# Optimization experiments

Measured on AMD Instinct MI355X. Metric: run time of the kernel, lower is better.

The kernel has to match this reference:

```python
import jax, jax.numpy as jnp
import numpy as np

EPS = 1e-6

def _rmsnorm(x, w):
    # RMSNorm in float32 as in the torch module, then rescale by weight
    xf = x.astype(jnp.float32)
    y = xf * jax.lax.rsqrt(jnp.mean(xf * xf, axis=-1, keepdims=True) + EPS)
    return y.astype(x.dtype) * w

def setup_inputs() -> dict:
    key = jax.random.key(0)
    k0, k1, k2 = jax.random.split(key, 3)
    B, T, C = 2, 1024, 256
    x = jax.random.normal(k0, (B, T, C), jnp.float32)
    w_qkv = jax.random.normal(k1, (3 * C, C), jnp.float32) / np.float32(np.sqrt(C))
    w_proj = jax.random.normal(k2, (C, C), jnp.float32) / np.float32(np.sqrt(C))
    qn_w = jnp.ones((2,), jnp.float32)
    kn_w = jnp.ones((2,), jnp.float32)
    return {"x": x, "w_qkv": w_qkv, "w_proj": w_proj, "qn_w": qn_w, "kn_w": kn_w}

def reference(x, w_qkv, w_proj, qn_w, kn_w):
    B, T, C = x.shape
    HD = 2                      # head_dim forced to 2 by GPTConfig invariant
    H = C // HD                 # n_head = n_embd // 2
    qkv = x @ w_qkv.T           # (B, T, 3C); Linear has bias=False
    q, k, v = jnp.split(qkv, 3, axis=-1)
    heads = lambda t: t.reshape(B, T, H, HD).transpose(0, 2, 1, 3)  # (B,H,T,2)
    q = _rmsnorm(heads(q), qn_w)
    k = _rmsnorm(heads(k), kn_w)
    v = heads(v)
    scale = np.float32(1.0 / np.sqrt(HD))
    att = jnp.einsum('bhtd,bhsd->bhts', q, k) * scale   # (B,H,T,T)
    causal = jnp.tril(jnp.ones((T, T), bool))
    att = jnp.where(causal, att, jnp.float32(-1e30))
    att = jax.nn.softmax(att, axis=-1)
    y = jnp.einsum('bhts,bhsd->bhtd', att, v)           # (B,H,T,2)
    y = y.transpose(0, 2, 1, 3).reshape(B, T, C)
    return y @ w_proj.T
```

## Files before the change

kernel.cpp:

```cpp
#include <hip/hip_runtime.h>

#define T_SEQ   1024
#define C_DIM   256
#define H_HEADS 128
#define NTOK    2048
#define BH      256
#define NBLK    1024

#define MAGIC1  0x1357ACE5u
#define MAGIC2  0x2468BD17u

typedef unsigned short u16;
typedef unsigned int   u32;
typedef __attribute__((ext_vector_type(8))) short bf16x8;
typedef __attribute__((ext_vector_type(4))) float f32x4;
typedef __attribute__((ext_vector_type(2))) float f32x2;
typedef __attribute__((ext_vector_type(2))) unsigned int u32x2;

__device__ __forceinline__ float bf2f(u16 u) {
  return __uint_as_float(((u32)u) << 16);
}
__device__ __forceinline__ u16 f2bf(float f) {
  u32 u = __float_as_uint(f);
  u32 r = u + 0x7fffu + ((u >> 16) & 1u);
  return (u16)(r >> 16);
}

__device__ __forceinline__ void stwt2(void* p, f32x2 v) {
  asm volatile("global_store_dwordx2 %0, %1, off sc0 sc1" :: "v"(p), "v"(v) : "memory");
}
__device__ __forceinline__ void stwt2u(void* p, u32x2 v) {
  asm volatile("global_store_dwordx2 %0, %1, off sc0 sc1" :: "v"(p), "v"(v) : "memory");
}

__device__ __forceinline__ bf16x8 ldsf(const u16* plane, int row, int kk) {
  int off = (row * 128 + kk * 2) ^ ((row & 7) << 4);
  return *(const bf16x8*)((const char*)plane + off);
}
__device__ __forceinline__ void cvt_store(float4 g, u16* hp, int lo_u16,
                                          int r, int c4) {
  ushort4 h4, l4;
  h4.x = f2bf(g.x); l4.x = f2bf(g.x - bf2f(h4.x));
  h4.y = f2bf(g.y); l4.y = f2bf(g.y - bf2f(h4.y));
  h4.z = f2bf(g.z); l4.z = f2bf(g.z - bf2f(h4.z));
  h4.w = f2bf(g.w); l4.w = f2bf(g.w - bf2f(h4.w));
  int off = (r * 128 + c4 * 2) ^ ((r & 7) << 4);
  *(ushort4*)((char*)hp + off) = h4;
  *(ushort4*)((char*)(hp + lo_u16) + off) = l4;
}

#define AG __HIP_MEMORY_SCOPE_AGENT
__device__ __forceinline__ void slot_set(u32* s, u32 v) {
  __hip_atomic_store(s, v, __ATOMIC_RELAXED, AG);
}
__device__ __forceinline__ u32 slot_get(const u32* s) {
  return __hip_atomic_load(s, __ATOMIC_RELAXED, AG);
}

__device__ __forceinline__ void attn_unit(
    char* smem, const float* __restrict__ q, const float* __restrict__ kk,
    const float* __restrict__ vv, u32* __restrict__ yP,
    int head, int g, int tid, int lane, int w)
{
  float4* skA = (float4*)smem;
  float4* skB = (float4*)(smem + 8192);
  float (*red)[256][3] = (float (*)[256][3])(smem + 16384);

  const int qb = g * 256;
  const int S  = qb + 256;

  {
    const float4* kh = (const float4*)(kk + head * (T_SEQ * 2));
    const float4* vh = (const float4*)(vv + head * (T_SEQ * 2));
    for (int i = tid; i < (S >> 1); i += 256) {
      float4 k4 = kh[i];
      float4 v4 = vh[i];
      skA[i] = make_float4(k4.x, k4.z, k4.y, k4.w);
      skB[i] = make_float4(v4.x, v4.z, v4.y, v4.w);
    }
  }

  const float LS = 0.70710678118f * 1.44269504089f;
  f32x2 qxb[4], qyb[4];
  int   tq[4];
#pragma unroll
  for (int j = 0; j < 4; ++j) {
    int t = qb + j * 64 + lane;
    tq[j] = t;
    float2 qv = *(const float2*)&q[(head * T_SEQ + t) * 2];
    float sx = qv.x * LS, sy = qv.y * LS;
    qxb[j] = (f32x2){sx, sx};
    qyb[j] = (f32x2){sy, sy};
  }
  __syncthreads();

  f32x2 denp[4] = {}, nxp[4] = {}, nyp[4] = {};

  const int cbp = qb >> 3;
  const int p0 = w * cbp, p1 = p0 + cbp;
  for (int p = p0; p < p1; p += 4) {
    float4 A0 = skA[p],     V0 = skB[p];
    float4 A1 = skA[p + 1], V1 = skB[p + 1];
    float4 A2 = skA[p + 2], V2 = skB[p + 2];
    float4 A3 = skA[p + 3], V3 = skB[p + 3];
#pragma unroll
    for (int u = 0; u < 4; ++u) {
      float4 A = (u == 0) ? A0 : (u == 1) ? A1 : (u == 2) ? A2 : A3;
      float4 V = (u == 0) ? V0 : (u == 1) ? V1 : (u == 2) ? V2 : V3;
      f32x2 kx = {A.x, A.y}, ky = {A.z, A.w};
      f32x2 vx = {V.x, V.y}, vy = {V.z, V.w};
#pragma unroll
      for (int j = 0; j < 4; ++j) {
        f32x2 sp = __builtin_elementwise_fma(qxb[j], kx, qyb[j] * ky);
        f32x2 ep = { __builtin_amdgcn_exp2f(sp.x), __builtin_amdgcn_exp2f(sp.y) };
        denp[j] += ep;
        nxp[j] = __builtin_elementwise_fma(ep, vx, nxp[j]);
        nyp[j] = __builtin_elementwise_fma(ep, vy, nyp[j]);
      }
    }
  }
  const int dp0 = (qb >> 1) + w * 32;
  for (int p = dp0; p < dp0 + 32; p += 4) {
    float4 A0 = skA[p],     V0 = skB[p];
    float4 A1 = skA[p + 1], V1 = skB[p + 1];
    float4 A2 = skA[p + 2], V2 = skB[p + 2];
    float4 A3 = skA[p + 3], V3 = skB[p + 3];
#pragma unroll
    for (int u = 0; u < 4; ++u) {
      float4 A = (u == 0) ? A0 : (u == 1) ? A1 : (u == 2) ? A2 : A3;
      float4 V = (u == 0) ? V0 : (u == 1) ? V1 : (u == 2) ? V2 : V3;
      f32x2 kx = {A.x, A.y}, ky = {A.z, A.w};
      f32x2 vx = {V.x, V.y}, vy = {V.z, V.w};
      const int s0 = 2 * (p + u);
#pragma unroll
      for (int j = 0; j < 4; ++j) {
        f32x2 sp = __builtin_elementwise_fma(qxb[j], kx, qyb[j] * ky);
        f32x2 ep = { __builtin_amdgcn_exp2f(sp.x), __builtin_amdgcn_exp2f(sp.y) };
        ep.x = (s0     <= tq[j]) ? ep.x : 0.f;
        ep.y = (s0 + 1 <= tq[j]) ? ep.y : 0.f;
        denp[j] += ep;
        nxp[j] = __builtin_elementwise_fma(ep, vx, nxp[j]);
        nyp[j] = __builtin_elementwise_fma(ep, vy, nyp[j]);
      }
    }
  }

#pragma unroll
  for (int j = 0; j < 4; ++j) {
    red[w][j * 64 + lane][0] = denp[j].x + denp[j].y;
    red[w][j * 64 + lane][1] = nxp[j].x + nxp[j].y;
    red[w][j * 64 + lane][2] = nyp[j].x + nyp[j].y;
  }
  __syncthreads();

  float dd = 0.f, ax = 0.f, ay = 0.f;
#pragma unroll
  for (int ww = 0; ww < 4; ++ww) {
    dd += red[ww][tid][0];
    ax += red[ww][tid][1];
    ay += red[ww][tid][2];
  }
  float inv = 1.f / dd;
  float ox = ax * inv, oy = ay * inv;
  u32 hx = f2bf(ox), hy = f2bf(oy);
  float rx = ox - bf2f((u16)hx), ry = oy - bf2f((u16)hy);
  u32x2 e = { hx | (hy << 16), (u32)f2bf(rx) | ((u32)f2bf(ry) << 16) };
  stwt2u(yP + ((size_t)head * T_SEQ + qb + tid) * 2, e);
}

__global__ __launch_bounds__(256, 4) void k_fused(
    const float* __restrict__ x, const float* __restrict__ wqkv,
    const float* __restrict__ wproj,
    const float* __restrict__ qnw, const float* __restrict__ knw,
    float* __restrict__ out,
    u32* __restrict__ slots1,
    u32* __restrict__ slotsY,
    float* __restrict__ q, float* __restrict__ kk, float* __restrict__ vv,
    u32* __restrict__ yP)
{
  __shared__ __align__(16) char smem[28672];

  const int tid  = threadIdx.x;
  const int blk  = blockIdx.x;
  const int lane = tid & 63;
  const int w    = tid >> 6;

  if (blk < 768) {
    u16* L = (u16*)smem;
    const int bx   = blk & 63, by = blk >> 6;
    const int row0 = bx * 32, col0 = by * 64;
    const int fr   = lane & 15;
    const int ko   = (lane >> 4) * 8;

    f32x4 acc[2] = {};
    float4 rx[2], rw[4];

    auto LOADR = [&](int kc) {
#pragma unroll
      for (int it = 0; it < 2; ++it) {
        int idx = it * 256 + tid;
        rx[it] = *(const float4*)&x[(row0 + (idx >> 4)) * C_DIM + kc * 64 + (idx & 15) * 4];
      }
#pragma unroll
      for (int it = 0; it < 4; ++it) {
        int idx = it * 256 + tid;
        rw[it] = *(const float4*)&wqkv[(col0 + (idx >> 4)) * C_DIM + kc * 64 + (idx & 15) * 4];
      }
    };

    LOADR(0);
    for (int kc = 0; kc < 4; ++kc) {
#pragma unroll
      for (int it = 0; it < 2; ++it) {
        int idx = it * 256 + tid;
        cvt_store(rx[it], L, 2048, idx >> 4, (idx & 15) * 4);
      }
#pragma unroll
      for (int it = 0; it < 4; ++it) {
        int idx = it * 256 + tid;
        cvt_store(rw[it], L + 4096, 4096, idx >> 4, (idx & 15) * 4);
      }
      __syncthreads();
      if (kc < 3) LOADR(kc + 1);
#pragma unroll
      for (int ks = 0; ks < 2; ++ks) {
        const int kk2 = ks * 32 + ko;
        bf16x8 bhi = ldsf(L + 4096, w * 16 + fr, kk2);
        bf16x8 blo = ldsf(L + 8192, w * 16 + fr, kk2);
#pragma unroll
        for (int rt = 0; rt < 2; ++rt) {
          bf16x8 ahi = ldsf(L,        rt * 16 + fr, kk2);
          bf16x8 alo = ldsf(L + 2048, rt * 16 + fr, kk2);
          acc[rt] = __builtin_amdgcn_mfma_f32_16x16x32_bf16(alo, bhi, acc[rt], 0, 0, 0);
          acc[rt] = __builtin_amdgcn_mfma_f32_16x16x32_bf16(ahi, blo, acc[rt], 0, 0, 0);
          acc[rt] = __builtin_amdgcn_mfma_f32_16x16x32_bf16(ahi, bhi, acc[rt], 0, 0, 0);
        }
      }
      __syncthreads();
    }

    const int sec = col0 >> 8;
    const int cg  = col0 + w * 16 + fr;
    const int d   = cg & 1;
    const float wn = (sec == 0) ? qnw[d] : (sec == 1) ? knw[d] : 1.f;
    float* sf = (float*)smem;
    const int cl = w * 16 + fr;

#pragma unroll
    for (int rt = 0; rt < 2; ++rt) {
#pragma unroll
      for (int i = 0; i < 4; ++i) {
        float val = acc[rt][i];
        if (sec < 2) {
          float pv = __shfl_xor(val, 1);
          float rr = rsqrtf(0.5f * (val * val + pv * pv) + 1e-6f);
          val = val * rr * wn;
        }
        int tl = rt * 16 + (lane >> 4) * 4 + i;
        sf[tl * 66 + cl] = val;
      }
    }
    __syncthreads();

    float* dst = (sec == 0) ? q : (sec == 1) ? kk : vv;
    const int b  = row0 >> 10, t0 = row0 & 1023;
    const int h0 = (col0 & 255) >> 1;
#pragma unroll
    for (int it = 0; it < 4; ++it) {
      int seg = w * 8 + it * 2 + (lane >> 5);
      int w2  = lane & 31;
      f32x2 v2 = { sf[w2 * 66 + seg * 2], sf[w2 * 66 + seg * 2 + 1] };
      stwt2(dst + ((size_t)((b * H_HEADS + h0 + seg)) * T_SEQ + t0 + w2) * 2, v2);
    }

    asm volatile("s_waitcnt vmcnt(0)" ::: "memory");
    __syncthreads();
    if (tid == 0) slot_set(slots1 + blk, MAGIC1);
  }

  {
    int g, head;
    if (blk >= 768)      { g = 3; head = blk - 768; }
    else if (blk < 256)  { g = 2; head = blk; }
    else if (blk < 512)  { g = 1; head = blk - 256; }
    else                 { g = 0; head = blk - 512; }

    const int b   = head >> 7;
    const int hq  = (head & 127) >> 5;
    const int h   = head & 127;
    const int kvn = 8 * (g + 1);
    const int qlo = g * 8;

    if (w == 0) {
      int guard = 0;
      for (;;) {
        bool ok = true;
        if (lane < 32) {
          if (lane < kvn) {
            int bxk = b * 32 + lane;
            ok &= (slot_get(slots1 + (4 + hq) * 64 + bxk) == MAGIC1);
            ok &= (slot_get(slots1 + (8 + hq) * 64 + bxk) == MAGIC1);
          }
        } else if (lane - 32 < 8) {
          int bxq = b * 32 + qlo + (lane - 32);
          ok &= (slot_get(slots1 + hq * 64 + bxq) == MAGIC1);
        }
        if (__all(ok)) break;
        __builtin_amdgcn_s_sleep(8);
        if (++guard > (1 << 20)) break;
      }
    }
    __builtin_amdgcn_fence(__ATOMIC_ACQUIRE, "workgroup");
    __syncthreads();

    attn_unit(smem, q, kk, vv, yP, head, g, tid, lane, w);
    asm volatile("s_waitcnt vmcnt(0)" ::: "memory");
    __syncthreads();
    if (tid == 0) slot_set(slotsY + (b * 4 + g) * 128 + h, MAGIC2);
  }

  if (blk >= 256 && blk < 768) {
    const int blkp = blk - 256;
    u16* L = (u16*)smem;
    const int bx   = blkp & 63, by = blkp >> 6;
    const int row0 = bx * 32, col0 = by * 32;
    const int b    = row0 >> 10, t0 = row0 & 1023;
    const int gs   = t0 >> 8;
    const int fr   = lane & 15;
    const int ko   = (lane >> 4) * 8;
    const int ar   = (w >> 1) * 16 + fr;
    const int br   = (w & 1) * 16 + fr;
    const int tl_  = tid & 31, hb = tid >> 5;

    f32x4 acc = {};
    float4 rw[2];
    u32x2  ry[4];

    auto LOADW = [&](int kc) {
#pragma unroll
      for (int it = 0; it < 2; ++it) {
        int idx = it * 256 + tid;
        rw[it] = *(const float4*)&wproj[(col0 + (idx >> 4)) * C_DIM + kc * 64 + (idx & 15) * 4];
      }
    };
    auto LOADY = [&](int kc) {
#pragma unroll
      for (int j = 0; j < 4; ++j) {
        int h = hb * 4 + j;
        ry[j] = *(const u32x2*)(yP + ((size_t)(b * H_HEADS + kc * 32 + h) * T_SEQ + t0 + tl_) * 2);
      }
    };

    LOADW(0);
    if (w == 0) {
      const u32* sy = slotsY + (b * 4 + gs) * 128;
      int guard = 0;
      for (;;) {
        bool ok = (slot_get(sy + lane) == MAGIC2) &
                  (slot_get(sy + 64 + lane) == MAGIC2);
        if (__all(ok)) break;
        __builtin_amdgcn_s_sleep(8);
        if (++guard > (1 << 20)) break;
      }
    }
    __builtin_amdgcn_fence(__ATOMIC_ACQUIRE, "workgroup");
    __syncthreads();

    LOADY(0);
    for (int kc = 0; kc < 4; ++kc) {
#pragma unroll
      for (int j = 0; j < 4; ++j) {
        int h = hb * 4 + j;
        int off = (tl_ * 128 + h * 4) ^ ((tl_ & 7) << 4);
        *(u32*)((char*)L + off)        = ry[j].x;
        *(u32*)((char*)L + 4096 + off) = ry[j].y;
      }
#pragma unroll
      for (int it = 0; it < 2; ++it) {
        int idx = it * 256 + tid;
        cvt_store(rw[it], L + 4096, 2048, idx >> 4, (idx & 15) * 4);
      }
      __syncthreads();
      if (kc < 3) { LOADW(kc + 1); LOADY(kc + 1); }
#pragma unroll
      for (int ks = 0; ks < 2; ++ks) {
        const int kk2 = ks * 32 + ko;
        bf16x8 bhi = ldsf(L + 4096, br, kk2);
        bf16x8 blo = ldsf(L + 6144, br, kk2);
        bf16x8 ahi = ldsf(L,        ar, kk2);
        bf16x8 alo = ldsf(L + 2048, ar, kk2);
        acc = __builtin_amdgcn_mfma_f32_16x16x32_bf16(alo, bhi, acc, 0, 0, 0);
        acc = __builtin_amdgcn_mfma_f32_16x16x32_bf16(ahi, blo, acc, 0, 0, 0);
        acc = __builtin_amdgcn_mfma_f32_16x16x32_bf16(ahi, bhi, acc, 0, 0, 0);
      }
      __syncthreads();
    }

    const int cg = col0 + (w & 1) * 16 + fr;
#pragma unroll
    for (int i = 0; i < 4; ++i) {
      int n = row0 + (w >> 1) * 16 + (lane >> 4) * 4 + i;
      out[n * C_DIM + cg] = acc[i];
    }
  }
}

extern "C" void kernel_launch(void* const* d_in, const int* in_sizes, int n_in,
                              void* d_out, int out_size, void* d_ws, size_t ws_size,
                              hipStream_t stream) {
  const float* x     = (const float*)d_in[0];
  const float* wqkv  = (const float*)d_in[1];
  const float* wproj = (const float*)d_in[2];
  const float* qnw   = (const float*)d_in[3];
  const float* knw   = (const float*)d_in[4];

  char* p = (char*)d_ws;
  u32* slots1 = (u32*)p;  p += 768 * 4;
  u32* slotsY = (u32*)p;  p += 1024 * 4;
  p = (char*)d_ws + 8192;
  float* q  = (float*)p;  p += (size_t)BH * T_SEQ * 2 * 4;
  float* kk = (float*)p;  p += (size_t)BH * T_SEQ * 2 * 4;
  float* vv = (float*)p;  p += (size_t)BH * T_SEQ * 2 * 4;
  u32* yP  = (u32*)p;     p += (size_t)BH * T_SEQ * 2 * 4;

  k_fused<<<NBLK, 256, 0, stream>>>(x, wqkv, wproj, qnw, knw, (float*)d_out,
                                    slots1, slotsY, q, kk, vv, yP);
}
```

Before: 110.4 us.

## Make inter-block dependency waits finer-grained and use packed bf16 conversion

The attention stage now waits on each 256-key chunk of K/V readiness separately and loads that chunk into shared memory before processing it, so compute can start before all producer blocks finish. The projection stage waits per 32-head group of attention outputs instead of all 128 heads before starting. Manual bf16 rounding is replaced by the hardware packed v_cvt_pk_bf16_f32 instruction. This adds more polls and barriers per block and moves the prefetch of the next chunk after the MFMA work, which reduces overlap of loads with compute.

```diff
diff --git a/kernel.cpp b/kernel.cpp
--- a/kernel.cpp
+++ b/kernel.cpp
@@ -20,10 +20,11 @@
 __device__ __forceinline__ float bf2f(u16 u) {
   return __uint_as_float(((u32)u) << 16);
 }
-__device__ __forceinline__ u16 f2bf(float f) {
-  u32 u = __float_as_uint(f);
-  u32 r = u + 0x7fffu + ((u >> 16) & 1u);
-  return (u16)(r >> 16);
+
+__device__ __forceinline__ u32 cvtpk(float a, float b) {
+  u32 r;
+  asm("v_cvt_pk_bf16_f32 %0, %1, %2" : "=v"(r) : "v"(a), "v"(b));
+  return r;
 }
 
 __device__ __forceinline__ void stwt2(void* p, f32x2 v) {
@@ -39,14 +40,14 @@
 }
 __device__ __forceinline__ void cvt_store(float4 g, u16* hp, int lo_u16,
                                           int r, int c4) {
-  ushort4 h4, l4;
-  h4.x = f2bf(g.x); l4.x = f2bf(g.x - bf2f(h4.x));
-  h4.y = f2bf(g.y); l4.y = f2bf(g.y - bf2f(h4.y));
-  h4.z = f2bf(g.z); l4.z = f2bf(g.z - bf2f(h4.z));
-  h4.w = f2bf(g.w); l4.w = f2bf(g.w - bf2f(h4.w));
+  u32 h01 = cvtpk(g.x, g.y), h23 = cvtpk(g.z, g.w);
+  float hx = __uint_as_float(h01 << 16), hy = __uint_as_float(h01 & 0xFFFF0000u);
+  float hz = __uint_as_float(h23 << 16), hw = __uint_as_float(h23 & 0xFFFF0000u);
+  u32 l01 = cvtpk(g.x - hx, g.y - hy), l23 = cvtpk(g.z - hz, g.w - hw);
   int off = (r * 128 + c4 * 2) ^ ((r & 7) << 4);
-  *(ushort4*)((char*)hp + off) = h4;
-  *(ushort4*)((char*)(hp + lo_u16) + off) = l4;
+  u32x2 hv = {h01, h23}, lv = {l01, l23};
+  *(u32x2*)((char*)hp + off) = hv;
+  *(u32x2*)((char*)(hp + lo_u16) + off) = lv;
 }
 
 #define AG __HIP_MEMORY_SCOPE_AGENT
@@ -58,7 +59,8 @@
 }
 
 __device__ __forceinline__ void attn_unit(
-    char* smem, const float* __restrict__ q, const float* __restrict__ kk,
+    char* smem, const u32* __restrict__ slots1,
+    const float* __restrict__ q, const float* __restrict__ kk,
     const float* __restrict__ vv, u32* __restrict__ yP,
     int head, int g, int tid, int lane, int w)
 {
@@ -67,18 +69,25 @@
   float (*red)[256][3] = (float (*)[256][3])(smem + 16384);
 
   const int qb = g * 256;
-  const int S  = qb + 256;
-
-  {
-    const float4* kh = (const float4*)(kk + head * (T_SEQ * 2));
-    const float4* vh = (const float4*)(vv + head * (T_SEQ * 2));
-    for (int i = tid; i < (S >> 1); i += 256) {
-      float4 k4 = kh[i];
-      float4 v4 = vh[i];
-      skA[i] = make_float4(k4.x, k4.z, k4.y, k4.w);
-      skB[i] = make_float4(v4.x, v4.z, v4.y, v4.w);
-    }
-  }
+  const int b  = head >> 7;
+  const int hq = (head & 127) >> 5;
+
+  const float4* kh = (const float4*)(kk + head * (T_SEQ * 2));
+  const float4* vh = (const float4*)(vv + head * (T_SEQ * 2));
+
+  if (w == 0) {
+    int guard = 0;
+    for (;;) {
+      bool ok = true;
+      if (lane < 8)
+        ok = (slot_get(slots1 + hq * 64 + b * 32 + g * 8 + lane) == MAGIC1);
+      if (__all(ok)) break;
+      __builtin_amdgcn_s_sleep(8);
+      if (++guard > (1 << 20)) break;
+    }
+  }
+  __builtin_amdgcn_fence(__ATOMIC_ACQUIRE, "workgroup");
+  __syncthreads();
 
   const float LS = 0.70710678118f * 1.44269504089f;
   f32x2 qxb[4], qyb[4];
@@ -92,55 +101,85 @@
     qxb[j] = (f32x2){sx, sx};
     qyb[j] = (f32x2){sy, sy};
   }
-  __syncthreads();
 
   f32x2 denp[4] = {}, nxp[4] = {}, nyp[4] = {};
 
-  const int cbp = qb >> 3;
-  const int p0 = w * cbp, p1 = p0 + cbp;
-  for (int p = p0; p < p1; p += 4) {
-    float4 A0 = skA[p],     V0 = skB[p];
-    float4 A1 = skA[p + 1], V1 = skB[p + 1];
-    float4 A2 = skA[p + 2], V2 = skB[p + 2];
-    float4 A3 = skA[p + 3], V3 = skB[p + 3];
-#pragma unroll
-    for (int u = 0; u < 4; ++u) {
-      float4 A = (u == 0) ? A0 : (u == 1) ? A1 : (u == 2) ? A2 : A3;
-      float4 V = (u == 0) ? V0 : (u == 1) ? V1 : (u == 2) ? V2 : V3;
-      f32x2 kx = {A.x, A.y}, ky = {A.z, A.w};
-      f32x2 vx = {V.x, V.y}, vy = {V.z, V.w};
-#pragma unroll
-      for (int j = 0; j < 4; ++j) {
-        f32x2 sp = __builtin_elementwise_fma(qxb[j], kx, qyb[j] * ky);
-        f32x2 ep = { __builtin_amdgcn_exp2f(sp.x), __builtin_amdgcn_exp2f(sp.y) };
-        denp[j] += ep;
-        nxp[j] = __builtin_elementwise_fma(ep, vx, nxp[j]);
-        nyp[j] = __builtin_elementwise_fma(ep, vy, nyp[j]);
-      }
-    }
-  }
-  const int dp0 = (qb >> 1) + w * 32;
-  for (int p = dp0; p < dp0 + 32; p += 4) {
-    float4 A0 = skA[p],     V0 = skB[p];
-    float4 A1 = skA[p + 1], V1 = skB[p + 1];
-    float4 A2 = skA[p + 2], V2 = skB[p + 2];
-    float4 A3 = skA[p + 3], V3 = skB[p + 3];
-#pragma unroll
-    for (int u = 0; u < 4; ++u) {
-      float4 A = (u == 0) ? A0 : (u == 1) ? A1 : (u == 2) ? A2 : A3;
-      float4 V = (u == 0) ? V0 : (u == 1) ? V1 : (u == 2) ? V2 : V3;
-      f32x2 kx = {A.x, A.y}, ky = {A.z, A.w};
-      f32x2 vx = {V.x, V.y}, vy = {V.z, V.w};
-      const int s0 = 2 * (p + u);
-#pragma unroll
-      for (int j = 0; j < 4; ++j) {
-        f32x2 sp = __builtin_elementwise_fma(qxb[j], kx, qyb[j] * ky);
-        f32x2 ep = { __builtin_amdgcn_exp2f(sp.x), __builtin_amdgcn_exp2f(sp.y) };
-        ep.x = (s0     <= tq[j]) ? ep.x : 0.f;
-        ep.y = (s0 + 1 <= tq[j]) ? ep.y : 0.f;
-        denp[j] += ep;
-        nxp[j] = __builtin_elementwise_fma(ep, vx, nxp[j]);
-        nyp[j] = __builtin_elementwise_fma(ep, vy, nyp[j]);
+  for (int c = 0; c <= g; ++c) {
+    if (w == 0) {
+      int guard = 0;
+      for (;;) {
+        bool ok = true;
+        if (lane < 8)
+          ok = (slot_get(slots1 + (4 + hq) * 64 + b * 32 + c * 8 + lane) == MAGIC1);
+        else if (lane < 16)
+          ok = (slot_get(slots1 + (8 + hq) * 64 + b * 32 + c * 8 + (lane - 8)) == MAGIC1);
+        if (__all(ok)) break;
+        __builtin_amdgcn_s_sleep(8);
+        if (++guard > (1 << 20)) break;
+      }
+    }
+    __builtin_amdgcn_fence(__ATOMIC_ACQUIRE, "workgroup");
+    __syncthreads();
+
+    {
+      int idx = c * 128 + (tid & 127);
+      if (tid < 128) {
+        float4 k4 = kh[idx];
+        skA[idx] = make_float4(k4.x, k4.z, k4.y, k4.w);
+      } else {
+        float4 v4 = vh[idx];
+        skB[idx] = make_float4(v4.x, v4.z, v4.y, v4.w);
+      }
+    }
+    __syncthreads();
+
+    const int p0 = c * 128 + w * 32;
+    if (c < g) {
+      for (int p = p0; p < p0 + 32; p += 4) {
+        float4 A0 = skA[p],     V0 = skB[p];
+        float4 A1 = skA[p + 1], V1 = skB[p + 1];
+        float4 A2 = skA[p + 2], V2 = skB[p + 2];
+        float4 A3 = skA[p + 3], V3 = skB[p + 3];
+#pragma unroll
+        for (int u = 0; u < 4; ++u) {
+          float4 A = (u == 0) ? A0 : (u == 1) ? A1 : (u == 2) ? A2 : A3;
+          float4 V = (u == 0) ? V0 : (u == 1) ? V1 : (u == 2) ? V2 : V3;
+          f32x2 kx = {A.x, A.y}, ky = {A.z, A.w};
+          f32x2 vx = {V.x, V.y}, vy = {V.z, V.w};
+#pragma unroll
+          for (int j = 0; j < 4; ++j) {
+            f32x2 sp = __builtin_elementwise_fma(qxb[j], kx, qyb[j] * ky);
+            f32x2 ep = { __builtin_amdgcn_exp2f(sp.x), __builtin_amdgcn_exp2f(sp.y) };
+            denp[j] += ep;
+            nxp[j] = __builtin_elementwise_fma(ep, vx, nxp[j]);
+            nyp[j] = __builtin_elementwise_fma(ep, vy, nyp[j]);
+          }
+        }
+      }
+    } else {
+      for (int p = p0; p < p0 + 32; p += 4) {
+        float4 A0 = skA[p],     V0 = skB[p];
+        float4 A1 = skA[p + 1], V1 = skB[p + 1];
+        float4 A2 = skA[p + 2], V2 = skB[p + 2];
+        float4 A3 = skA[p + 3], V3 = skB[p + 3];
+#pragma unroll
+        for (int u = 0; u < 4; ++u) {
+          float4 A = (u == 0) ? A0 : (u == 1) ? A1 : (u == 2) ? A2 : A3;
+          float4 V = (u == 0) ? V0 : (u == 1) ? V1 : (u == 2) ? V2 : V3;
+          f32x2 kx = {A.x, A.y}, ky = {A.z, A.w};
+          f32x2 vx = {V.x, V.y}, vy = {V.z, V.w};
+          const int s0 = 2 * (p + u);
+#pragma unroll
+          for (int j = 0; j < 4; ++j) {
+            f32x2 sp = __builtin_elementwise_fma(qxb[j], kx, qyb[j] * ky);
+            f32x2 ep = { __builtin_amdgcn_exp2f(sp.x), __builtin_amdgcn_exp2f(sp.y) };
+            ep.x = (s0     <= tq[j]) ? ep.x : 0.f;
+            ep.y = (s0 + 1 <= tq[j]) ? ep.y : 0.f;
+            denp[j] += ep;
+            nxp[j] = __builtin_elementwise_fma(ep, vx, nxp[j]);
+            nyp[j] = __builtin_elementwise_fma(ep, vy, nyp[j]);
+          }
+        }
       }
     }
   }
@@ -162,9 +201,10 @@
   }
   float inv = 1.f / dd;
   float ox = ax * inv, oy = ay * inv;
-  u32 hx = f2bf(ox), hy = f2bf(oy);
-  float rx = ox - bf2f((u16)hx), ry = oy - bf2f((u16)hy);
-  u32x2 e = { hx | (hy << 16), (u32)f2bf(rx) | ((u32)f2bf(ry) << 16) };
+  u32 hP = cvtpk(ox, oy);
+  float hx_f = __uint_as_float(hP << 16), hy_f = __uint_as_float(hP & 0xFFFF0000u);
+  u32 lP = cvtpk(ox - hx_f, oy - hy_f);
+  u32x2 e = { hP, lP };
   stwt2u(yP + ((size_t)head * T_SEQ + qb + tid) * 2, e);
 }
 
@@ -285,35 +325,10 @@
     else if (blk < 512)  { g = 1; head = blk - 256; }
     else                 { g = 0; head = blk - 512; }
 
-    const int b   = head >> 7;
-    const int hq  = (head & 127) >> 5;
-    const int h   = head & 127;
-    const int kvn = 8 * (g + 1);
-    const int qlo = g * 8;
-
-    if (w == 0) {
-      int guard = 0;
-      for (;;) {
-        bool ok = true;
-        if (lane < 32) {
-          if (lane < kvn) {
-            int bxk = b * 32 + lane;
-            ok &= (slot_get(slots1 + (4 + hq) * 64 + bxk) == MAGIC1);
-            ok &= (slot_get(slots1 + (8 + hq) * 64 + bxk) == MAGIC1);
-          }
-        } else if (lane - 32 < 8) {
-          int bxq = b * 32 + qlo + (lane - 32);
-          ok &= (slot_get(slots1 + hq * 64 + bxq) == MAGIC1);
-        }
-        if (__all(ok)) break;
-        __builtin_amdgcn_s_sleep(8);
-        if (++guard > (1 << 20)) break;
-      }
-    }
-    __builtin_amdgcn_fence(__ATOMIC_ACQUIRE, "workgroup");
-    __syncthreads();
-
-    attn_unit(smem, q, kk, vv, yP, head, g, tid, lane, w);
+    const int b = head >> 7;
+    const int h = head & 127;
+
+    attn_unit(smem, slots1, q, kk, vv, yP, head, g, tid, lane, w);
     asm volatile("s_waitcnt vmcnt(0)" ::: "memory");
     __syncthreads();
     if (tid == 0) slot_set(slotsY + (b * 4 + g) * 128 + h, MAGIC2);
@@ -331,6 +346,7 @@
     const int ar   = (w >> 1) * 16 + fr;
     const int br   = (w & 1) * 16 + fr;
     const int tl_  = tid & 31, hb = tid >> 5;
+    const u32* sy  = slotsY + (b * 4 + gs) * 128;
 
     f32x4 acc = {};
     float4 rw[2];
@@ -346,32 +362,33 @@
     auto LOADY = [&](int kc) {
 #pragma unroll
       for (int j = 0; j < 4; ++j) {
-        int h = hb * 4 + j;
-        ry[j] = *(const u32x2*)(yP + ((size_t)(b * H_HEADS + kc * 32 + h) * T_SEQ + t0 + tl_) * 2);
+        int hh = hb * 4 + j;
+        ry[j] = *(const u32x2*)(yP + ((size_t)(b * H_HEADS + kc * 32 + hh) * T_SEQ + t0 + tl_) * 2);
       }
     };
+    auto POLLH = [&](int kc) {
+      if (w == 0) {
+        int guard = 0;
+        for (;;) {
+          bool ok = true;
+          if (lane < 32) ok = (slot_get(sy + kc * 32 + lane) == MAGIC2);
+          if (__all(ok)) break;
+          __builtin_amdgcn_s_sleep(8);
+          if (++guard > (1 << 20)) break;
+        }
+      }
+      __builtin_amdgcn_fence(__ATOMIC_ACQUIRE, "workgroup");
+    };
 
     LOADW(0);
-    if (w == 0) {
-      const u32* sy = slotsY + (b * 4 + gs) * 128;
-      int guard = 0;
-      for (;;) {
-        bool ok = (slot_get(sy + lane) == MAGIC2) &
-                  (slot_get(sy + 64 + lane) == MAGIC2);
-        if (__all(ok)) break;
-        __builtin_amdgcn_s_sleep(8);
-        if (++guard > (1 << 20)) break;
-      }
-    }
-    __builtin_amdgcn_fence(__ATOMIC_ACQUIRE, "workgroup");
-    __syncthreads();
-
+    POLLH(0);
+    __syncthreads();
     LOADY(0);
     for (int kc = 0; kc < 4; ++kc) {
 #pragma unroll
       for (int j = 0; j < 4; ++j) {
-        int h = hb * 4 + j;
-        int off = (tl_ * 128 + h * 4) ^ ((tl_ & 7) << 4);
+        int hh = hb * 4 + j;
+        int off = (tl_ * 128 + hh * 4) ^ ((tl_ & 7) << 4);
         *(u32*)((char*)L + off)        = ry[j].x;
         *(u32*)((char*)L + 4096 + off) = ry[j].y;
       }
@@ -381,7 +398,7 @@
         cvt_store(rw[it], L + 4096, 2048, idx >> 4, (idx & 15) * 4);
       }
       __syncthreads();
-      if (kc < 3) { LOADW(kc + 1); LOADY(kc + 1); }
+      if (kc < 3) POLLH(kc + 1);
 #pragma unroll
       for (int ks = 0; ks < 2; ++ks) {
         const int kk2 = ks * 32 + ko;
@@ -394,6 +411,7 @@
         acc = __builtin_amdgcn_mfma_f32_16x16x32_bf16(ahi, bhi, acc, 0, 0, 0);
       }
       __syncthreads();
+      if (kc < 3) { LOADW(kc + 1); LOADY(kc + 1); }
     }
 
     const int cg = col0 + (w & 1) * 16 + fr;
```

Result: no change. 110.8 us (+0.4%).

## Read K/V directly from global in attention and use packed bf16 conversion

Applied to the files above, without the earlier changes.

The attention unit no longer stages K and V into shared memory. Each wave reads float4 pairs straight from global memory (through the caches) and reorders components in registers, which removes the staging loop and a barrier. The shared buffer shrinks accordingly, which may raise occupancy. Separately, the software round-to-nearest bf16 split is replaced with the hardware v_cvt_pk_bf16_f32 packed conversion, cutting ALU work in the hi/lo splitting. In exchange, each wave now issues redundant global loads that rely on cache hits, and load latency sits directly in the compute loop.

```diff
diff --git a/kernel.cpp b/kernel.cpp
--- a/kernel.cpp
+++ b/kernel.cpp
@@ -17,13 +17,10 @@
 typedef __attribute__((ext_vector_type(2))) float f32x2;
 typedef __attribute__((ext_vector_type(2))) unsigned int u32x2;
 
-__device__ __forceinline__ float bf2f(u16 u) {
-  return __uint_as_float(((u32)u) << 16);
-}
-__device__ __forceinline__ u16 f2bf(float f) {
-  u32 u = __float_as_uint(f);
-  u32 r = u + 0x7fffu + ((u >> 16) & 1u);
-  return (u16)(r >> 16);
+__device__ __forceinline__ u32 cvtpk(float a, float b) {
+  u32 r;
+  asm("v_cvt_pk_bf16_f32 %0, %1, %2" : "=v"(r) : "v"(a), "v"(b));
+  return r;
 }
 
 __device__ __forceinline__ void stwt2(void* p, f32x2 v) {
@@ -39,14 +36,14 @@
 }
 __device__ __forceinline__ void cvt_store(float4 g, u16* hp, int lo_u16,
                                           int r, int c4) {
-  ushort4 h4, l4;
-  h4.x = f2bf(g.x); l4.x = f2bf(g.x - bf2f(h4.x));
-  h4.y = f2bf(g.y); l4.y = f2bf(g.y - bf2f(h4.y));
-  h4.z = f2bf(g.z); l4.z = f2bf(g.z - bf2f(h4.z));
-  h4.w = f2bf(g.w); l4.w = f2bf(g.w - bf2f(h4.w));
+  u32 h01 = cvtpk(g.x, g.y), h23 = cvtpk(g.z, g.w);
+  float hx = __uint_as_float(h01 << 16), hy = __uint_as_float(h01 & 0xFFFF0000u);
+  float hz = __uint_as_float(h23 << 16), hw = __uint_as_float(h23 & 0xFFFF0000u);
+  u32 l01 = cvtpk(g.x - hx, g.y - hy), l23 = cvtpk(g.z - hz, g.w - hw);
   int off = (r * 128 + c4 * 2) ^ ((r & 7) << 4);
-  *(ushort4*)((char*)hp + off) = h4;
-  *(ushort4*)((char*)(hp + lo_u16) + off) = l4;
+  u32x2 hv = {h01, h23}, lv = {l01, l23};
+  *(u32x2*)((char*)hp + off) = hv;
+  *(u32x2*)((char*)(hp + lo_u16) + off) = lv;
 }
 
 #define AG __HIP_MEMORY_SCOPE_AGENT
@@ -62,23 +59,11 @@
     const float* __restrict__ vv, u32* __restrict__ yP,
     int head, int g, int tid, int lane, int w)
 {
-  float4* skA = (float4*)smem;
-  float4* skB = (float4*)(smem + 8192);
-  float (*red)[256][3] = (float (*)[256][3])(smem + 16384);
+  float (*red)[256][3] = (float (*)[256][3])smem;
 
   const int qb = g * 256;
-  const int S  = qb + 256;
-
-  {
-    const float4* kh = (const float4*)(kk + head * (T_SEQ * 2));
-    const float4* vh = (const float4*)(vv + head * (T_SEQ * 2));
-    for (int i = tid; i < (S >> 1); i += 256) {
-      float4 k4 = kh[i];
-      float4 v4 = vh[i];
-      skA[i] = make_float4(k4.x, k4.z, k4.y, k4.w);
-      skB[i] = make_float4(v4.x, v4.z, v4.y, v4.w);
-    }
-  }
+  const float4* kh = (const float4*)(kk + head * (T_SEQ * 2));
+  const float4* vh = (const float4*)(vv + head * (T_SEQ * 2));
 
   const float LS = 0.70710678118f * 1.44269504089f;
   f32x2 qxb[4], qyb[4];
@@ -92,23 +77,22 @@
     qxb[j] = (f32x2){sx, sx};
     qyb[j] = (f32x2){sy, sy};
   }
-  __syncthreads();
 
   f32x2 denp[4] = {}, nxp[4] = {}, nyp[4] = {};
 
   const int cbp = qb >> 3;
   const int p0 = w * cbp, p1 = p0 + cbp;
   for (int p = p0; p < p1; p += 4) {
-    float4 A0 = skA[p],     V0 = skB[p];
-    float4 A1 = skA[p + 1], V1 = skB[p + 1];
-    float4 A2 = skA[p + 2], V2 = skB[p + 2];
-    float4 A3 = skA[p + 3], V3 = skB[p + 3];
+    float4 A0 = kh[p],     V0 = vh[p];
+    float4 A1 = kh[p + 1], V1 = vh[p + 1];
+    float4 A2 = kh[p + 2], V2 = vh[p + 2];
+    float4 A3 = kh[p + 3], V3 = vh[p + 3];
 #pragma unroll
     for (int u = 0; u < 4; ++u) {
       float4 A = (u == 0) ? A0 : (u == 1) ? A1 : (u == 2) ? A2 : A3;
       float4 V = (u == 0) ? V0 : (u == 1) ? V1 : (u == 2) ? V2 : V3;
-      f32x2 kx = {A.x, A.y}, ky = {A.z, A.w};
-      f32x2 vx = {V.x, V.y}, vy = {V.z, V.w};
+      f32x2 kx = {A.x, A.z}, ky = {A.y, A.w};
+      f32x2 vx = {V.x, V.z}, vy = {V.y, V.w};
 #pragma unroll
       for (int j = 0; j < 4; ++j) {
         f32x2 sp = __builtin_elementwise_fma(qxb[j], kx, qyb[j] * ky);
@@ -121,16 +105,16 @@
   }
   const int dp0 = (qb >> 1) + w * 32;
   for (int p = dp0; p < dp0 + 32; p += 4) {
-    float4 A0 = skA[p],     V0 = skB[p];
-    float4 A1 = skA[p + 1], V1 = skB[p + 1];
-    float4 A2 = skA[p + 2], V2 = skB[p + 2];
-    float4 A3 = skA[p + 3], V3 = skB[p + 3];
+    float4 A0 = kh[p],     V0 = vh[p];
+    float4 A1 = kh[p + 1], V1 = vh[p + 1];
+    float4 A2 = kh[p + 2], V2 = vh[p + 2];
+    float4 A3 = kh[p + 3], V3 = vh[p + 3];
 #pragma unroll
     for (int u = 0; u < 4; ++u) {
       float4 A = (u == 0) ? A0 : (u == 1) ? A1 : (u == 2) ? A2 : A3;
       float4 V = (u == 0) ? V0 : (u == 1) ? V1 : (u == 2) ? V2 : V3;
-      f32x2 kx = {A.x, A.y}, ky = {A.z, A.w};
-      f32x2 vx = {V.x, V.y}, vy = {V.z, V.w};
+      f32x2 kx = {A.x, A.z}, ky = {A.y, A.w};
+      f32x2 vx = {V.x, V.z}, vy = {V.y, V.w};
       const int s0 = 2 * (p + u);
 #pragma unroll
       for (int j = 0; j < 4; ++j) {
@@ -162,9 +146,10 @@
   }
   float inv = 1.f / dd;
   float ox = ax * inv, oy = ay * inv;
-  u32 hx = f2bf(ox), hy = f2bf(oy);
-  float rx = ox - bf2f((u16)hx), ry = oy - bf2f((u16)hy);
-  u32x2 e = { hx | (hy << 16), (u32)f2bf(rx) | ((u32)f2bf(ry) << 16) };
+  u32 hP = cvtpk(ox, oy);
+  float hx_f = __uint_as_float(hP << 16), hy_f = __uint_as_float(hP & 0xFFFF0000u);
+  u32 lP = cvtpk(ox - hx_f, oy - hy_f);
+  u32x2 e = { hP, lP };
   stwt2u(yP + ((size_t)head * T_SEQ + qb + tid) * 2, e);
 }
 
@@ -178,7 +163,7 @@
     float* __restrict__ q, float* __restrict__ kk, float* __restrict__ vv,
     u32* __restrict__ yP)
 {
-  __shared__ __align__(16) char smem[28672];
+  __shared__ __align__(16) char smem[24576];
 
   const int tid  = threadIdx.x;
   const int blk  = blockIdx.x;
@@ -346,8 +331,8 @@
     auto LOADY = [&](int kc) {
 #pragma unroll
       for (int j = 0; j < 4; ++j) {
-        int h = hb * 4 + j;
-        ry[j] = *(const u32x2*)(yP + ((size_t)(b * H_HEADS + kc * 32 + h) * T_SEQ + t0 + tl_) * 2);
+        int hh = hb * 4 + j;
+        ry[j] = *(const u32x2*)(yP + ((size_t)(b * H_HEADS + kc * 32 + hh) * T_SEQ + t0 + tl_) * 2);
       }
     };
 
@@ -370,8 +355,8 @@
     for (int kc = 0; kc < 4; ++kc) {
 #pragma unroll
       for (int j = 0; j < 4; ++j) {
-        int h = hb * 4 + j;
-        int off = (tl_ * 128 + h * 4) ^ ((tl_ & 7) << 4);
+        int hh = hb * 4 + j;
+        int off = (tl_ * 128 + hh * 4) ^ ((tl_ & 7) << 4);
         *(u32*)((char*)L + off)        = ry[j].x;
         *(u32*)((char*)L + 4096 + off) = ry[j].y;
       }
```

After: 117.4 us. +6.4%, slower.
